# Kernel tuning notes

Measured on AMD Instinct MI355X. Metric: run time of the kernel, lower is better.

Reference implementation:

```python
import jax, jax.numpy as jnp
import numpy as np

NUM_HEADS = 16
HIDDEN = 1024
HEAD_DIM = HIDDEN // NUM_HEADS
B, S, D = 2, 2048, 1024


def setup_inputs() -> dict:
    key = jax.random.key(0)
    ks = jax.random.split(key, 7)
    scale = 1.0 / np.sqrt(D)
    return {
        "query": jax.random.normal(ks[0], (B, S, D), dtype=jnp.float32),
        "key": jax.random.normal(ks[1], (B, S, D), dtype=jnp.float32),
        "value": jax.random.normal(ks[2], (B, S, D), dtype=jnp.float32),
        "Wk_w": jax.random.normal(ks[3], (HIDDEN, D), dtype=jnp.float32) * scale,
        "Wk_b": jax.random.normal(ks[4], (HIDDEN,), dtype=jnp.float32) * scale,
        "Wv_w": jax.random.normal(ks[5], (HIDDEN, D), dtype=jnp.float32) * scale,
        "Wv_b": jax.random.normal(ks[6], (HIDDEN,), dtype=jnp.float32) * scale,
    }


def reference(query, key, value, Wk_w, Wk_b, Wv_w, Wv_b):
    # NOTE: in the original torch module, self.W_v is assigned twice, so the
    # SAME Linear (Wv) projects both key and value; Wk projects query.
    b, s, _ = query.shape

    def split_heads(x):  # [b,s,hidden] -> [b,h,s,hd]
        return x.reshape(b, s, NUM_HEADS, HEAD_DIM).transpose(0, 2, 1, 3)

    q = split_heads(query @ Wk_w.T + Wk_b)
    k = split_heads(key @ Wv_w.T + Wv_b)
    v = split_heads(value @ Wv_w.T + Wv_b)

    scores = jnp.einsum("bhqd,bhkd->bhqk", q, k) / jnp.sqrt(
        jnp.asarray(HEAD_DIM, dtype=q.dtype))
    probs = jax.nn.softmax(scores, axis=-1)
    out = jnp.einsum("bhqk,bhkd->bhqd", probs, v)
    return out.transpose(0, 2, 1, 3).reshape(b, s, NUM_HEADS * HEAD_DIM)
```

## Files before the change

### kernel.cpp

```cpp
#include <hip/hip_runtime.h>
#include <stdint.h>

typedef unsigned short u16;
typedef uint32_t u32;
typedef __bf16 bf16x8 __attribute__((ext_vector_type(8)));
typedef float f32x4 __attribute__((ext_vector_type(4)));
typedef float f32x16 __attribute__((ext_vector_type(16)));
typedef u16 u16x4 __attribute__((ext_vector_type(4)));
typedef u16 u16x8 __attribute__((ext_vector_type(8)));

#define XQ_OFF 0ul
#define XK_OFF 4194304ul
#define XV_OFF 8388608ul
#define WK_OFF 12582912ul
#define WV_OFF 13631488ul
#define Q_OFF  14680064ul
#define K_OFF  18874368ul
#define V_OFF  23068672ul

#define SCQ 0.18033688011112042f

#if __has_builtin(__builtin_amdgcn_exp2f)
#define EXP2F(x) __builtin_amdgcn_exp2f(x)
#else
#define EXP2F(x) exp2f(x)
#endif

__device__ __forceinline__ u16 f2bf(float f) {
  u32 u = __float_as_uint(f);
  u32 r = (u + 0x7fffu + ((u >> 16) & 1u)) >> 16;
  return (u16)r;
}

__device__ __forceinline__ u32 pk2(float a, float b) {
  typedef __bf16 bf2_t __attribute__((ext_vector_type(2)));
  typedef float f2_t __attribute__((ext_vector_type(2)));
  f2_t v; v[0] = a; v[1] = b;
  bf2_t h = __builtin_convertvector(v, bf2_t);
  union { bf2_t h; u32 u; } cv; cv.h = h; return cv.u;
}

__device__ __forceinline__ void load_lds16(const void* g, void* l) {
  __builtin_amdgcn_global_load_lds(
      (const __attribute__((address_space(1))) u32*)g,
      (__attribute__((address_space(3))) u32*)l, 16, 0, 0);
}

__device__ __forceinline__ u32 swz(u32 L) {
  return L ^ (((L >> 7) & 1u) << 4) ^ (((L >> 10) & 3u) << 5);
}

__global__ __launch_bounds__(256) void cvt_tile_kernel(
    const float* __restrict__ xq, const float* __restrict__ xk,
    const float* __restrict__ xv, const float* __restrict__ wk,
    const float* __restrict__ wv, u16* __restrict__ ws) {
  __shared__ u16 tile[4096];
  const int bid = blockIdx.x;
  const float* src; size_t dstbase; int rt, ktp;
  if (bid < 3072) {
    int m = bid >> 10, loc = bid & 1023;
    src = (m == 0) ? xq : (m == 1) ? xk : xv;
    dstbase = (size_t)m * 4194304ul;
    rt = loc >> 4; ktp = loc & 15;
  } else {
    int r2 = bid - 3072;
    int m = r2 >> 8, loc = r2 & 255;
    src = m ? wv : wk;
    dstbase = WK_OFF + (size_t)m * 1048576ul;
    rt = loc >> 4; ktp = loc & 15;
  }
  const int t = threadIdx.x;
  const int row0 = t >> 4, c = t & 15;
  const int k = c * 4;
  const float* s = src + (size_t)(rt * 64 + row0) * 1024ul + ktp * 64 + k;
#pragma unroll
  for (int i = 0; i < 4; ++i) {
    float4 v = *(const float4*)(s + (size_t)i * 16384ul);
    int row = row0 + i * 16;
    u32* p = (u32*)(tile + ((k >> 5) * 2048 + ((k >> 3) & 3) * 512 + row * 8 + (k & 7)));
    p[0] = pk2(v.x, v.y);
    p[1] = pk2(v.z, v.w);
  }
  __syncthreads();
  u16* dst = ws + dstbase + (size_t)(rt * 32 + ktp * 2) * 2048ul;
#pragma unroll
  for (int so = 0; so < 4096; so += 2048)
    *(u16x8*)(dst + so + t * 8) = *(const u16x8*)(tile + so + t * 8);
}

__global__ __launch_bounds__(256, 2) void proj_kernel(u16* __restrict__ ws,
                                                      const float* __restrict__ bk,
                                                      const float* __restrict__ bv) {
  const int proj = blockIdx.z;
  const int mtile = blockIdx.x;
  const int ntile = blockIdx.y;
  const u16* A = ws + (size_t)proj * 4194304ul;
  const u16* Bw = ws + ((proj == 0) ? WK_OFF : WV_OFF);
  const float* bias = (proj == 0) ? bk : bv;
  u16* outQ = ws + Q_OFF;
  u16* outK = ws + K_OFF;
  u16* outV = ws + V_OFF;

  const int t = threadIdx.x;
  const int w = t >> 6, lane = t & 63;
  const int wm = w >> 1, wn = w & 1;
  const int g = lane >> 4, c = lane & 15;

  __shared__ __align__(16) u16 smem[32768];

  const u16* Ag = A + (size_t)(2 * mtile) * 65536ul;
  const u16* Bg = Bw + (size_t)(2 * ntile) * 65536ul;
  const u32 t8 = (u32)t * 8u;
  const u32 so = swz((u32)t * 16u) >> 1;

  u32 poff[4];
#pragma unroll
  for (int mt = 0; mt < 4; ++mt)
    poff[mt] = swz((u32)((g << 10) | ((mt * 16 + c) << 4))) >> 1;

#define PSTAGE(buf, kt)                                            \
  do {                                                             \
    u16* bb = smem + (buf) * 8192;                                 \
    const size_t ko = (size_t)(kt) * 2048ul + so;                  \
    load_lds16(Ag + ko, bb + t8);                                  \
    load_lds16(Ag + 65536ul + ko, bb + 2048 + t8);                 \
    load_lds16(Bg + ko, bb + 4096 + t8);                           \
    load_lds16(Bg + 65536ul + ko, bb + 6144 + t8);                 \
  } while (0)

#define PFRAGS_MFMA(buf)                                                        \
  do {                                                                          \
    const u16* Ap = smem + (buf) * 8192 + wm * 2048;                            \
    const u16* Bp = smem + (buf) * 8192 + 4096 + wn * 2048;                     \
    bf16x8 af[4], bfv[4];                                                       \
    _Pragma("unroll") for (int mt = 0; mt < 4; ++mt)                            \
        af[mt] = *(const bf16x8*)(Ap + poff[mt]);                               \
    _Pragma("unroll") for (int nt = 0; nt < 4; ++nt)                            \
        bfv[nt] = *(const bf16x8*)(Bp + poff[nt]);                              \
    _Pragma("unroll") for (int mt = 0; mt < 4; ++mt)                            \
        _Pragma("unroll") for (int nt = 0; nt < 4; ++nt)                        \
            acc[mt][nt] = __builtin_amdgcn_mfma_f32_16x16x32_bf16(              \
                af[mt], bfv[nt], acc[mt][nt], 0, 0, 0);                         \
  } while (0)

  f32x4 acc[4][4];
#pragma unroll
  for (int mt = 0; mt < 4; ++mt)
#pragma unroll
    for (int nt = 0; nt < 4; ++nt) acc[mt][nt] = (f32x4){0.f, 0.f, 0.f, 0.f};

  PSTAGE(0, 0);
  PSTAGE(1, 1);
  PSTAGE(2, 2);
  PSTAGE(3, 3);

#pragma unroll 1
  for (int p = 0; p < 15; ++p) {
    asm volatile("s_waitcnt vmcnt(8)\n\ts_barrier" ::: "memory");
    const int b0 = (2 * p) & 3;
    PFRAGS_MFMA(b0);
    PFRAGS_MFMA(b0 + 1);
    __builtin_amdgcn_s_barrier();
    if (p < 14) {
      PSTAGE(b0, 2 * p + 4);
      PSTAGE(b0 + 1, 2 * p + 5);
    }
  }
  asm volatile("s_waitcnt vmcnt(0)\n\ts_barrier" ::: "memory");
  PFRAGS_MFMA(2);
  PFRAGS_MFMA(3);
#undef PSTAGE
#undef PFRAGS_MFMA

  const int m0 = mtile * 128 + wm * 64;
  const int n0 = ntile * 128 + wn * 64;
  if (proj == 2) {
#pragma unroll
    for (int nt = 0; nt < 4; ++nt) {
      const int col = n0 + nt * 16 + c;
      const float bvv = bias[col];
      const int h = col >> 6, d = col & 63;
#pragma unroll
      for (int mt = 0; mt < 4; ++mt) {
        const int mbase = m0 + mt * 16 + g * 4;
        const int b = mbase >> 11;
        const int bh = b * 16 + h;
        const int s = mbase & 2047;
        u16x4 pk;
#pragma unroll
        for (int r = 0; r < 4; ++r) pk[r] = f2bf(acc[mt][nt][r] + bvv);
        size_t idx = (size_t)bh * 131072ul + (size_t)(s >> 6) * 4096ul +
                     (size_t)((s & 63) >> 3) * 512ul + (size_t)d * 8ul + (size_t)(s & 7);
        *(u16x4*)(outV + idx) = pk;
      }
    }
  } else {
    __syncthreads();
    u16* Ew = smem + w * 4096;
#pragma unroll
    for (int nt = 0; nt < 4; ++nt) {
      const int d = nt * 16 + c;
      const float bvv = bias[n0 + nt * 16 + c];
#pragma unroll
      for (int mt = 0; mt < 4; ++mt) {
#pragma unroll
        for (int r = 0; r < 4; ++r) {
          const int srow = mt * 16 + g * 4 + r;
          float y = acc[mt][nt][r] + bvv;
          if (proj == 0) y *= SCQ;
          Ew[(d >> 3) * 512 + srow * 8 + (d & 7)] = f2bf(y);
        }
      }
    }
    __syncthreads();
    const int b = mtile >> 4;
    const int bh = b * 16 + ntile * 2 + wn;
    if (proj == 0) {
      u16* base = outQ + (size_t)bh * 131072ul + (size_t)(mtile & 15) * 8192ul + wm * 512;
#pragma unroll
      for (int i = 0; i < 8; ++i)
        *(u16x8*)(base + i * 1024 + lane * 8) = *(const u16x8*)(Ew + i * 512 + lane * 8);
    } else {
      u16* base = outK + (size_t)bh * 131072ul + (size_t)((mtile & 15) * 2 + wm) * 4096ul;
#pragma unroll
      for (int i = 0; i < 8; ++i)
        *(u16x8*)(base + i * 512 + lane * 8) = *(const u16x8*)(Ew + i * 512 + lane * 8);
    }
  }
}

__global__ __launch_bounds__(256, 2) void attn_kernel(const u16* __restrict__ ws,
                                                      float* __restrict__ out) {
  const int bh = blockIdx.x, qtile = blockIdx.y;
  const int b = bh >> 4, h = bh & 15;
  const int t = threadIdx.x, w = t >> 6, lane = t & 63;
  const int c32 = lane & 31, g2 = lane >> 5;

  __shared__ __align__(16) u16 Ks[3][4096];
  __shared__ __align__(16) u16 Vs[3][4096];

  const u16* Qg = ws + Q_OFF + (size_t)bh * 131072ul + (size_t)qtile * 8192ul;
  const u16* Kg = ws + K_OFF + (size_t)bh * 131072ul;
  const u16* Vg = ws + V_OFF + (size_t)bh * 131072ul;

  bf16x8 qf[4];
#pragma unroll
  for (int ks = 0; ks < 4; ++ks)
    qf[ks] = *(const bf16x8*)(Qg + (size_t)(ks * 2 + g2) * 1024ul +
                              (size_t)(w * 32 + c32) * 8ul);

  f32x16 O0, O1, Lacc;
#pragma unroll
  for (int i = 0; i < 16; ++i) { O0[i] = 0.f; O1[i] = 0.f; Lacc[i] = 0.f; }

#define STAGE_KV(buf, jj)                                        \
  do {                                                           \
    const u16* Kj = Kg + (size_t)(jj) * 4096ul;                  \
    const u16* Vj = Vg + (size_t)(jj) * 4096ul;                  \
    load_lds16(Kj + (size_t)t * 8ul, &Ks[buf][t * 8]);           \
    load_lds16(Kj + 2048ul + (size_t)t * 8ul, &Ks[buf][2048 + t * 8]); \
    load_lds16(Vj + (size_t)t * 8ul, &Vs[buf][t * 8]);           \
    load_lds16(Vj + 2048ul + (size_t)t * 8ul, &Vs[buf][2048 + t * 8]); \
  } while (0)

  STAGE_KV(0, 0);
  STAGE_KV(1, 1);

  int buf = 0;
#pragma unroll 1
  for (int j = 0; j < 32; ++j) {
    asm volatile("s_waitcnt vmcnt(4)\n\ts_barrier" ::: "memory");
    const u16* Kb = Ks[buf];
    const u16* Vb = Vs[buf];
    {
      int jc = (j + 2 < 32) ? j + 2 : 31;
      int sb = buf - 1; if (sb < 0) sb += 3;
      STAGE_KV(sb, jc);
    }

    f32x16 S0, S1;
#pragma unroll
    for (int i = 0; i < 16; ++i) { S0[i] = 0.f; S1[i] = 0.f; }
    __builtin_amdgcn_s_setprio(1);
#pragma unroll
    for (int ks = 0; ks < 4; ++ks) {
      bf16x8 kf0 = *(const bf16x8*)(Kb + (ks * 2 + g2) * 512 + c32 * 8);
      bf16x8 kf1 = *(const bf16x8*)(Kb + (ks * 2 + g2) * 512 + (32 + c32) * 8);
      S0 = __builtin_amdgcn_mfma_f32_32x32x16_bf16(kf0, qf[ks], S0, 0, 0, 0);
      S1 = __builtin_amdgcn_mfma_f32_32x32x16_bf16(kf1, qf[ks], S1, 0, 0, 0);
    }
    __builtin_amdgcn_s_setprio(0);

#pragma unroll
    for (int i = 0; i < 16; ++i) { S0[i] = EXP2F(S0[i]); S1[i] = EXP2F(S1[i]); }
    Lacc += S0;
    Lacc += S1;

    u32 pa[4][4];
#pragma unroll
    for (int half = 0; half < 2; ++half) {
      const f32x16& Sx = half ? S1 : S0;
#pragma unroll
      for (int sub = 0; sub < 2; ++sub) {
        const int rb = sub * 8;
        u32 q0 = pk2(Sx[rb + 0], Sx[rb + 1]);
        u32 q1 = pk2(Sx[rb + 2], Sx[rb + 3]);
        u32 q2 = pk2(Sx[rb + 4], Sx[rb + 5]);
        u32 q3 = pk2(Sx[rb + 6], Sx[rb + 7]);
        asm volatile("v_permlane32_swap_b32 %0, %1" : "+v"(q0), "+v"(q2));
        asm volatile("v_permlane32_swap_b32 %0, %1" : "+v"(q1), "+v"(q3));
        const int kstep = half * 2 + sub;
        pa[kstep][0] = q0; pa[kstep][1] = q1; pa[kstep][2] = q2; pa[kstep][3] = q3;
      }
    }

    __builtin_amdgcn_s_setprio(1);
#pragma unroll
    for (int kstep = 0; kstep < 4; ++kstep) {
      union { u32 u[4]; bf16x8 b; } pcv;
#pragma unroll
      for (int i = 0; i < 4; ++i) pcv.u[i] = pa[kstep][i];
      bf16x8 vf0 = *(const bf16x8*)(Vb + (kstep * 2 + g2) * 512 + c32 * 8);
      bf16x8 vf1 = *(const bf16x8*)(Vb + (kstep * 2 + g2) * 512 + (32 + c32) * 8);
      O0 = __builtin_amdgcn_mfma_f32_32x32x16_bf16(pcv.b, vf0, O0, 0, 0, 0);
      O1 = __builtin_amdgcn_mfma_f32_32x32x16_bf16(pcv.b, vf1, O1, 0, 0, 0);
    }
    __builtin_amdgcn_s_setprio(0);

    buf = (buf == 2) ? 0 : buf + 1;
  }
#undef STAGE_KV

  float lp = 0.f;
#pragma unroll
  for (int i = 0; i < 16; ++i) lp += Lacc[i];
  float lA = lp, lB = lp;
  asm volatile("v_permlane32_swap_b32 %0, %1" : "+v"(lA), "+v"(lB));
  const float Ltot = lA + lB;

  const int q0 = qtile * 128 + w * 32;
  float* outb = out + (size_t)(b * 2048 + q0) * 1024ul + h * 64 + c32;
#pragma unroll
  for (int r = 0; r < 16; ++r) {
    const int qr = (r & 3) + 8 * (r >> 2) + 4 * g2;
    int lv = __builtin_amdgcn_ds_bpermute(qr << 2, __float_as_int(Ltot));
    const float inv = 1.0f / __int_as_float(lv);
    float* rp = outb + (size_t)qr * 1024ul;
    rp[0] = O0[r] * inv;
    rp[32] = O1[r] * inv;
  }
}

extern "C" void kernel_launch(void* const* d_in, const int* in_sizes, int n_in,
                              void* d_out, int out_size, void* d_ws, size_t ws_size,
                              hipStream_t stream) {
  const float* q = (const float*)d_in[0];
  const float* k = (const float*)d_in[1];
  const float* v = (const float*)d_in[2];
  const float* wk = (const float*)d_in[3];
  const float* bk = (const float*)d_in[4];
  const float* wv = (const float*)d_in[5];
  const float* bv = (const float*)d_in[6];
  u16* ws = (u16*)d_ws;
  float* out = (float*)d_out;

  cvt_tile_kernel<<<3584, 256, 0, stream>>>(q, k, v, wk, wv, ws);
  proj_kernel<<<dim3(32, 8, 3), 256, 0, stream>>>(ws, bk, bv);
  attn_kernel<<<dim3(32, 16), 256, 0, stream>>>(ws, out);
}
```

Measured before the change: 172.9 us.

## Split attention KV sequence across two warp groups with in-block reduction

The attention kernel now launches 512 threads per block. Two groups of four warps each process half of the key/value sequence, with a separate double-buffered LDS pipeline per group instead of the previous triple buffer. The partial outputs and row sums are combined through shared memory before the final normalized store. This doubles the parallelism per query tile to hide latency better on a small grid of 512 blocks. The cost is a full vmcnt(0) wait each iteration, an extra LDS exchange and barrier at the end, and 64KB of LDS per block, which may limit occupancy.

Result: no change. 174.6 us (+1.0%).

```diff
diff --git a/kernel.cpp b/kernel.cpp
--- a/kernel.cpp
+++ b/kernel.cpp
@@ -229,54 +229,58 @@
   }
 }
 
-__global__ __launch_bounds__(256, 2) void attn_kernel(const u16* __restrict__ ws,
+__global__ __launch_bounds__(512, 4) void attn_kernel(u16* __restrict__ ws,
                                                       float* __restrict__ out) {
   const int bh = blockIdx.x, qtile = blockIdx.y;
   const int b = bh >> 4, h = bh & 15;
   const int t = threadIdx.x, w = t >> 6, lane = t & 63;
   const int c32 = lane & 31, g2 = lane >> 5;
-
-  __shared__ __align__(16) u16 Ks[3][4096];
-  __shared__ __align__(16) u16 Vs[3][4096];
+  const int hf = w >> 2;
+  const int wi = w & 3;
+
+  __shared__ __align__(16) u16 smemA[32768];
 
   const u16* Qg = ws + Q_OFF + (size_t)bh * 131072ul + (size_t)qtile * 8192ul;
-  const u16* Kg = ws + K_OFF + (size_t)bh * 131072ul;
-  const u16* Vg = ws + V_OFF + (size_t)bh * 131072ul;
+
+  const int hfs = t >> 8, tt = t & 255;
+  const u16* KgS = ws + K_OFF + (size_t)bh * 131072ul + (size_t)hfs * 65536ul;
+  const u16* VgS = ws + V_OFF + (size_t)bh * 131072ul + (size_t)hfs * 65536ul;
+  u16* kb0 = smemA + hfs * 2 * 4096;
+  u16* vb0 = smemA + 16384 + hfs * 2 * 4096;
+
+  const u16* Kb0 = smemA + hf * 2 * 4096;
+  const u16* Vb0 = smemA + 16384 + hf * 2 * 4096;
 
   bf16x8 qf[4];
 #pragma unroll
   for (int ks = 0; ks < 4; ++ks)
     qf[ks] = *(const bf16x8*)(Qg + (size_t)(ks * 2 + g2) * 1024ul +
-                              (size_t)(w * 32 + c32) * 8ul);
+                              (size_t)(wi * 32 + c32) * 8ul);
 
   f32x16 O0, O1, Lacc;
 #pragma unroll
   for (int i = 0; i < 16; ++i) { O0[i] = 0.f; O1[i] = 0.f; Lacc[i] = 0.f; }
 
-#define STAGE_KV(buf, jj)                                        \
-  do {                                                           \
-    const u16* Kj = Kg + (size_t)(jj) * 4096ul;                  \
-    const u16* Vj = Vg + (size_t)(jj) * 4096ul;                  \
-    load_lds16(Kj + (size_t)t * 8ul, &Ks[buf][t * 8]);           \
-    load_lds16(Kj + 2048ul + (size_t)t * 8ul, &Ks[buf][2048 + t * 8]); \
-    load_lds16(Vj + (size_t)t * 8ul, &Vs[buf][t * 8]);           \
-    load_lds16(Vj + 2048ul + (size_t)t * 8ul, &Vs[buf][2048 + t * 8]); \
+#define STAGE_KV(buf, jj)                                          \
+  do {                                                             \
+    const u16* Kj = KgS + (size_t)(jj) * 4096ul;                   \
+    const u16* Vj = VgS + (size_t)(jj) * 4096ul;                   \
+    u16* kb = kb0 + (buf) * 4096;                                  \
+    u16* vb = vb0 + (buf) * 4096;                                  \
+    load_lds16(Kj + (size_t)tt * 8ul, kb + tt * 8);                \
+    load_lds16(Kj + 2048ul + (size_t)tt * 8ul, kb + 2048 + tt * 8);\
+    load_lds16(Vj + (size_t)tt * 8ul, vb + tt * 8);                \
+    load_lds16(Vj + 2048ul + (size_t)tt * 8ul, vb + 2048 + tt * 8);\
   } while (0)
 
   STAGE_KV(0, 0);
-  STAGE_KV(1, 1);
-
-  int buf = 0;
+
 #pragma unroll 1
-  for (int j = 0; j < 32; ++j) {
-    asm volatile("s_waitcnt vmcnt(4)\n\ts_barrier" ::: "memory");
-    const u16* Kb = Ks[buf];
-    const u16* Vb = Vs[buf];
-    {
-      int jc = (j + 2 < 32) ? j + 2 : 31;
-      int sb = buf - 1; if (sb < 0) sb += 3;
-      STAGE_KV(sb, jc);
-    }
+  for (int j = 0; j < 16; ++j) {
+    asm volatile("s_waitcnt vmcnt(0)\n\ts_barrier" ::: "memory");
+    if (j < 15) STAGE_KV((j + 1) & 1, j + 1);
+    const u16* Kb = Kb0 + (j & 1) * 4096;
+    const u16* Vb = Vb0 + (j & 1) * 4096;
 
     f32x16 S0, S1;
 #pragma unroll
@@ -326,8 +330,6 @@
       O1 = __builtin_amdgcn_mfma_f32_32x32x16_bf16(pcv.b, vf1, O1, 0, 0, 0);
     }
     __builtin_amdgcn_s_setprio(0);
-
-    buf = (buf == 2) ? 0 : buf + 1;
   }
 #undef STAGE_KV
 
@@ -336,18 +338,31 @@
   for (int i = 0; i < 16; ++i) lp += Lacc[i];
   float lA = lp, lB = lp;
   asm volatile("v_permlane32_swap_b32 %0, %1" : "+v"(lA), "+v"(lB));
-  const float Ltot = lA + lB;
-
-  const int q0 = qtile * 128 + w * 32;
-  float* outb = out + (size_t)(b * 2048 + q0) * 1024ul + h * 64 + c32;
-#pragma unroll
-  for (int r = 0; r < 16; ++r) {
-    const int qr = (r & 3) + 8 * (r >> 2) + 4 * g2;
-    int lv = __builtin_amdgcn_ds_bpermute(qr << 2, __float_as_int(Ltot));
-    const float inv = 1.0f / __int_as_float(lv);
-    float* rp = outb + (size_t)qr * 1024ul;
-    rp[0] = O0[r] * inv;
-    rp[32] = O1[r] * inv;
+  float Ltot = lA + lB;
+
+  asm volatile("s_waitcnt lgkmcnt(0)" ::: "memory");
+  __syncthreads();
+  float* exch = (float*)smemA;
+  float* ex = exch + (size_t)(wi * 64 + lane) * 33ul;
+  if (hf == 1) {
+#pragma unroll
+    for (int i = 0; i < 16; ++i) { ex[i] = O0[i]; ex[16 + i] = O1[i]; }
+    ex[32] = Ltot;
+  }
+  __syncthreads();
+  if (hf == 0) {
+    const float Ltc = Ltot + ex[32];
+    const int q0 = qtile * 128 + wi * 32;
+    float* outb = out + (size_t)(b * 2048 + q0) * 1024ul + h * 64 + c32;
+#pragma unroll
+    for (int r = 0; r < 16; ++r) {
+      const int qr = (r & 3) + 8 * (r >> 2) + 4 * g2;
+      int lv = __builtin_amdgcn_ds_bpermute(qr << 2, __float_as_int(Ltc));
+      const float inv = 1.0f / __int_as_float(lv);
+      float* rp = outb + (size_t)qr * 1024ul;
+      rp[0] = (O0[r] + ex[r]) * inv;
+      rp[32] = (O1[r] + ex[16 + r]) * inv;
+    }
   }
 }
 
@@ -366,5 +381,5 @@
 
   cvt_tile_kernel<<<3584, 256, 0, stream>>>(q, k, v, wk, wv, ws);
   proj_kernel<<<dim3(32, 8, 3), 256, 0, stream>>>(ws, bk, bv);
-  attn_kernel<<<dim3(32, 16), 256, 0, stream>>>(ws, out);
-}
+  attn_kernel<<<dim3(32, 16), 512, 0, stream>>>(ws, out);
+}
```
